# Kernel optimization log

Measured on AMD Instinct MI355X. Metric: run time of the kernel, lower is better.

Reference implementation:

```python
import jax, jax.numpy as jnp
import numpy as np

B, N, D, H = 4, 4096, 1024, 16
DK = D // H  # 64


def setup_inputs() -> dict:
    key = jax.random.key(0)
    ks = jax.random.split(key, 11)
    s_in = 1.0 / np.sqrt(D)
    s_out = 1.0 / np.sqrt(H * DK)
    return {
        "query": jax.random.normal(ks[0], (B, N, D), jnp.float32),
        "key": jax.random.normal(ks[1], (B, N, D), jnp.float32),
        "value": jax.random.normal(ks[2], (B, N, D), jnp.float32),
        # stacked per-head Linear weights (torch Linear: y = x @ W.T + b)
        "Wq": jax.random.uniform(ks[3], (H, DK, D), jnp.float32, -s_in, s_in),
        "bq": jax.random.uniform(ks[4], (H, DK), jnp.float32, -s_in, s_in),
        "Wk": jax.random.uniform(ks[5], (H, DK, D), jnp.float32, -s_in, s_in),
        "bk": jax.random.uniform(ks[6], (H, DK), jnp.float32, -s_in, s_in),
        "Wv": jax.random.uniform(ks[7], (H, DK, D), jnp.float32, -s_in, s_in),
        "bv": jax.random.uniform(ks[8], (H, DK), jnp.float32, -s_in, s_in),
        "Wo": jax.random.uniform(ks[9], (D, H * DK), jnp.float32, -s_out, s_out),
        "bo": jax.random.uniform(ks[10], (D,), jnp.float32, -s_out, s_out),
    }


def reference(query, key, value, Wq, bq, Wk, bk, Wv, bv, Wo, bo):
    b, n, _ = query.shape
    # batched per-head projections: [b,h,n,d_k]
    q = jnp.einsum('bnd,hkd->bhnk', query, Wq) + bq[None, :, None, :]
    k = jnp.einsum('bnd,hkd->bhnk', key, Wk) + bk[None, :, None, :]
    v = jnp.einsum('bnd,hkd->bhnk', value, Wv) + bv[None, :, None, :]
    # linear dot-product attention (faithful: scale by batch**-0.5)
    q = jax.nn.softmax(q, axis=-1) * (b ** -0.5)
    k = jax.nn.softmax(k, axis=-2)  # softmax over sequence dim
    ctx = jnp.einsum('bhnd,bhne->bhde', k, v)      # [b,h,d_k,d_v]
    attn = jnp.einsum('bhnd,bhde->bhne', q, ctx)   # [b,h,n,d_v]
    # concat heads along last dim: [b,n,h*d_v]
    concat = attn.transpose(0, 2, 1, 3).reshape(b, n, -1)
    return concat @ Wo.T + bo
```

## Files before the change

kernel.cpp:

```cpp
#include <hip/hip_runtime.h>
#include <hip/hip_bf16.h>
#include <stdint.h>

#define B_  4
#define N_  4096
#define D_  1024
#define H_  16
#define DK_ 64
#define M_  (B_ * N_)

typedef __attribute__((ext_vector_type(8))) short  short8;
typedef __attribute__((ext_vector_type(4))) float  f32x4;

__device__ __forceinline__ uint16_t f2bf(float f) {
  union { float f; uint32_t u; } v; v.f = f;
  uint32_t r = v.u + 0x7FFF + ((v.u >> 16) & 1);
  return (uint16_t)(r >> 16);
}
__device__ __forceinline__ uint32_t f2bf2(float lo, float hi) {
  return (uint32_t)f2bf(lo) | ((uint32_t)f2bf(hi) << 16);
}
__device__ __forceinline__ float bf2f(uint16_t u) {
  union { uint32_t u; float f; } v; v.u = ((uint32_t)u) << 16;
  return v.f;
}

__device__ __forceinline__ void gload_lds16(const void* g, void* l) {
  __builtin_amdgcn_global_load_lds((const __attribute__((address_space(1))) void*)g,
                                   (__attribute__((address_space(3))) void*)l, 16, 0, 0);
}

#define S_BARRIER() __builtin_amdgcn_s_barrier()
#define FENCE_LGKM0() asm volatile("s_waitcnt lgkmcnt(0)" ::: "memory")
#define FENCE_VM4()   asm volatile("s_waitcnt vmcnt(4) lgkmcnt(0)" ::: "memory")
#define FENCE_VM0()   asm volatile("s_waitcnt vmcnt(0) lgkmcnt(0)" ::: "memory")

__global__ __launch_bounds__(256) void pack_bf16_kernel(
    const float* q, const float* k, const float* v,
    const float* wq, const float* wk, const float* wv, const float* wo,
    uint16_t* xq, uint16_t* xk, uint16_t* xv,
    uint16_t* bwq, uint16_t* bwk, uint16_t* bwv, uint16_t* bwo)
{
  const float* src; uint16_t* dst; int count;
  switch (blockIdx.y) {
    case 0: src = q;  dst = xq;  count = M_ * D_; break;
    case 1: src = k;  dst = xk;  count = M_ * D_; break;
    case 2: src = v;  dst = xv;  count = M_ * D_; break;
    case 3: src = wq; dst = bwq; count = D_ * D_; break;
    case 4: src = wk; dst = bwk; count = D_ * D_; break;
    case 5: src = wv; dst = bwv; count = D_ * D_; break;
    default: src = wo; dst = bwo; count = D_ * D_; break;
  }
  int base = blockIdx.x * 4096;
  if (base >= count) return;
  int t = threadIdx.x;
#pragma unroll
  for (int j = 0; j < 2; ++j) {
    int idx = base + j * 2048 + t * 8;
    float4 f0 = *(const float4*)(src + idx);
    float4 f1 = *(const float4*)(src + idx + 4);
    uint4 o;
    o.x = f2bf2(f0.x, f0.y); o.y = f2bf2(f0.z, f0.w);
    o.z = f2bf2(f1.x, f1.y); o.w = f2bf2(f1.z, f1.w);
    *(uint4*)(dst + idx) = o;
  }
}

template<int EPI, int BATCHW>
__global__ __launch_bounds__(512, 2) void gemm256_kernel(
    const uint16_t* __restrict__ A,
    const uint16_t* __restrict__ W,
    const float* __restrict__ bias,
    void* __restrict__ C,
    float* __restrict__ pm, float* __restrict__ ps)
{
  extern __shared__ uint16_t smem[];
  uint16_t* As = smem;
  uint16_t* Bs = smem + 32768;
  float* sredm = (float*)(smem + 65536);
  float* sreds = sredm + 512;

  const int tid = threadIdx.x;
  const int w = tid >> 6, l = tid & 63;
  const int lr = l & 15, kg = l >> 4;
  const int wr = w >> 2, wc = w & 3;
  const int rsw = lr & 7;
  const int srcswz = ((tid >> 3) & 7) << 4;

  const int flat = blockIdx.y * 4 + blockIdx.x;
  const int swzf = (flat & 7) * 32 + (flat >> 3);
  const int brow = swzf >> 2, bcol = swzf & 3;
  const int NT = 16;

  const uint16_t* Wb = BATCHW ? (W + (size_t)(brow >> 4) * ((size_t)D_ * D_)) : W;
  const int arow0 = brow * 256, bcrow0 = bcol * 256;

  f32x4 acc[8][4];
#pragma unroll
  for (int i = 0; i < 8; ++i)
#pragma unroll
    for (int j = 0; j < 4; ++j) acc[i][j] = (f32x4){0.f, 0.f, 0.f, 0.f};

  auto stage_half = [&](const uint16_t* g, int row0, int kt, uint16_t* ldst, int h) {
#pragma unroll
    for (int i = 0; i < 2; ++i) {
      int lin = h * 16384 + i * 8192 + tid * 16;
      int src = lin ^ srcswz;
      const uint16_t* gp = g + (size_t)(row0 + (src >> 7)) * D_ + kt * 64 + ((src & 127) >> 1);
      uint16_t* lp = ldst + h * 8192 + i * 4096 + w * 512;
      gload_lds16(gp, lp);
    }
  };
  auto rdfrag = [&](const uint16_t* tile, int row, int ks) -> short8 {
    return *(const short8*)(tile + row * 64 + ((((ks << 2) | kg) ^ rsw) << 3));
  };

  stage_half(A, arow0, 0, As, 0);  stage_half(A, arow0, 0, As, 1);
  stage_half(Wb, bcrow0, 0, Bs, 0); stage_half(Wb, bcrow0, 0, Bs, 1);
  stage_half(A, arow0, 1, As + 16384, 0); stage_half(A, arow0, 1, As + 16384, 1);
  FENCE_VM4();
  S_BARRIER();

  short8 af0[4][2], af1[4][2], bfr[2][2];
  for (int t = 0; t < NT; ++t) {
    const int p = t & 1;
    uint16_t* Ap = As + p * 16384;
    uint16_t* Bp = Bs + p * 16384;
    uint16_t* An = As + (p ^ 1) * 16384;
    uint16_t* Bn = Bs + (p ^ 1) * 16384;

#pragma unroll
    for (int mi = 0; mi < 4; ++mi)
#pragma unroll
      for (int ks = 0; ks < 2; ++ks)
        af0[mi][ks] = rdfrag(Ap, wr * 128 + mi * 16 + lr, ks);
#pragma unroll
    for (int ni = 0; ni < 2; ++ni)
#pragma unroll
      for (int ks = 0; ks < 2; ++ks)
        bfr[ni][ks] = rdfrag(Bp, wc * 64 + ni * 16 + lr, ks);
    if (t + 1 < NT) stage_half(Wb, bcrow0, t + 1, Bn, 0);
    S_BARRIER();
    __builtin_amdgcn_s_setprio(1);
#pragma unroll
    for (int mi = 0; mi < 4; ++mi)
#pragma unroll
      for (int ni = 0; ni < 2; ++ni)
#pragma unroll
        for (int ks = 0; ks < 2; ++ks)
          acc[mi][ni] = __builtin_amdgcn_mfma_f32_16x16x32_bf16(af0[mi][ks], bfr[ni][ks], acc[mi][ni], 0, 0, 0);
    __builtin_amdgcn_s_setprio(0);
    FENCE_LGKM0();
    S_BARRIER();

#pragma unroll
    for (int mi = 0; mi < 4; ++mi)
#pragma unroll
      for (int ks = 0; ks < 2; ++ks)
        af1[mi][ks] = rdfrag(Ap, wr * 128 + 64 + mi * 16 + lr, ks);
#pragma unroll
    for (int ni = 0; ni < 2; ++ni)
#pragma unroll
      for (int ks = 0; ks < 2; ++ks)
        bfr[ni][ks] = rdfrag(Bp, wc * 64 + (ni + 2) * 16 + lr, ks);
    if (t + 1 < NT) stage_half(Wb, bcrow0, t + 1, Bn, 1);
    S_BARRIER();
    __builtin_amdgcn_s_setprio(1);
#pragma unroll
    for (int mi = 0; mi < 4; ++mi)
#pragma unroll
      for (int ni = 0; ni < 2; ++ni)
#pragma unroll
        for (int ks = 0; ks < 2; ++ks)
          acc[mi + 4][ni + 2] = __builtin_amdgcn_mfma_f32_16x16x32_bf16(af1[mi][ks], bfr[ni][ks], acc[mi + 4][ni + 2], 0, 0, 0);
    __builtin_amdgcn_s_setprio(0);
    FENCE_LGKM0();
    S_BARRIER();

#pragma unroll
    for (int ni = 0; ni < 2; ++ni)
#pragma unroll
      for (int ks = 0; ks < 2; ++ks)
        bfr[ni][ks] = rdfrag(Bp, wc * 64 + ni * 16 + lr, ks);
    if (t + 2 < NT) stage_half(A, arow0, t + 2, Ap, 0);
    S_BARRIER();
    __builtin_amdgcn_s_setprio(1);
#pragma unroll
    for (int mi = 0; mi < 4; ++mi)
#pragma unroll
      for (int ni = 0; ni < 2; ++ni)
#pragma unroll
        for (int ks = 0; ks < 2; ++ks)
          acc[mi + 4][ni] = __builtin_amdgcn_mfma_f32_16x16x32_bf16(af1[mi][ks], bfr[ni][ks], acc[mi + 4][ni], 0, 0, 0);
    __builtin_amdgcn_s_setprio(0);
    FENCE_LGKM0();
    S_BARRIER();

#pragma unroll
    for (int ni = 0; ni < 2; ++ni)
#pragma unroll
      for (int ks = 0; ks < 2; ++ks)
        bfr[ni][ks] = rdfrag(Bp, wc * 64 + (ni + 2) * 16 + lr, ks);
    if (t + 2 < NT) stage_half(A, arow0, t + 2, Ap, 1);
    S_BARRIER();
    __builtin_amdgcn_s_setprio(1);
#pragma unroll
    for (int mi = 0; mi < 4; ++mi)
#pragma unroll
      for (int ni = 0; ni < 2; ++ni)
#pragma unroll
        for (int ks = 0; ks < 2; ++ks)
          acc[mi][ni + 2] = __builtin_amdgcn_mfma_f32_16x16x32_bf16(af0[mi][ks], bfr[ni][ks], acc[mi][ni + 2], 0, 0, 0);
    __builtin_amdgcn_s_setprio(0);
    if (t <= 13)      { FENCE_VM4(); }
    else if (t == 14) { FENCE_VM0(); }
    else              { FENCE_LGKM0(); }
    S_BARRIER();
  }

  if (EPI == 2) {
    float bv[4];
#pragma unroll
    for (int ni = 0; ni < 4; ++ni) bv[ni] = bias[bcol * 256 + wc * 64 + ni * 16 + lr];
#pragma unroll
    for (int mi = 0; mi < 8; ++mi) {
#pragma unroll
      for (int j = 0; j < 4; ++j) {
        float v0 = acc[mi][0][j] + bv[0];
        float v1 = acc[mi][1][j] + bv[1];
        float v2 = acc[mi][2][j] + bv[2];
        float v3 = acc[mi][3][j] + bv[3];
        float m = fmaxf(fmaxf(v0, v1), fmaxf(v2, v3));
#pragma unroll
        for (int o = 1; o < 16; o <<= 1) m = fmaxf(m, __shfl_xor(m, o));
        float p0 = __expf(v0 - m), p1 = __expf(v1 - m);
        float p2 = __expf(v2 - m), p3 = __expf(v3 - m);
        float s = (p0 + p1) + (p2 + p3);
#pragma unroll
        for (int o = 1; o < 16; o <<= 1) s += __shfl_xor(s, o);
        float sc = 0.5f / s;
        int row = brow * 256 + wr * 128 + mi * 16 + kg * 4 + j;
        uint16_t* out = (uint16_t*)C + (size_t)row * D_ + bcol * 256 + wc * 64 + lr;
        out[0]  = f2bf(p0 * sc);
        out[16] = f2bf(p1 * sc);
        out[32] = f2bf(p2 * sc);
        out[48] = f2bf(p3 * sc);
      }
    }
  } else if (EPI == 3) {
#pragma unroll
    for (int ni = 0; ni < 4; ++ni) {
      int coll = wc * 64 + ni * 16 + lr;
      int col = bcol * 256 + coll;
      float bvn = bias[col];
      float vals[8][4];
      float m = -1e30f;
#pragma unroll
      for (int mi = 0; mi < 8; ++mi)
#pragma unroll
        for (int j = 0; j < 4; ++j) {
          float val = acc[mi][ni][j] + bvn;
          vals[mi][j] = val;
          m = fmaxf(m, val);
          int row = brow * 256 + wr * 128 + mi * 16 + kg * 4 + j;
          ((uint16_t*)C)[(size_t)row * D_ + col] = f2bf(val);
        }
      m = fmaxf(m, __shfl_xor(m, 16));
      m = fmaxf(m, __shfl_xor(m, 32));
      float s = 0.f;
#pragma unroll
      for (int mi = 0; mi < 8; ++mi)
#pragma unroll
        for (int j = 0; j < 4; ++j) s += __expf(vals[mi][j] - m);
      s += __shfl_xor(s, 16);
      s += __shfl_xor(s, 32);
      if (l < 16) {
        sredm[wr * 256 + coll] = m;
        sreds[wr * 256 + coll] = s;
      }
    }
    __syncthreads();
    if (tid < 256) {
      float m0 = sredm[tid], m1 = sredm[256 + tid];
      float s0 = sreds[tid], s1 = sreds[256 + tid];
      float m = fmaxf(m0, m1);
      float s = s0 * __expf(m0 - m) + s1 * __expf(m1 - m);
      pm[(size_t)brow * D_ + bcol * 256 + tid] = m;
      ps[(size_t)brow * D_ + bcol * 256 + tid] = s;
    }
  } else {
#pragma unroll
    for (int mi = 0; mi < 8; ++mi) {
#pragma unroll
      for (int ni = 0; ni < 4; ++ni) {
        int col = bcol * 256 + wc * 64 + ni * 16 + lr;
        float bv = bias[col];
#pragma unroll
        for (int j = 0; j < 4; ++j) {
          int row = brow * 256 + wr * 128 + mi * 16 + kg * 4 + j;
          float val = acc[mi][ni][j] + bv;
          if (EPI == 1) ((float*)C)[(size_t)row * D_ + col] = val;
          else          ((uint16_t*)C)[(size_t)row * D_ + col] = f2bf(val);
        }
      }
    }
  }
}

__global__ __launch_bounds__(256) void colstats_final_kernel(
    const float* __restrict__ pm, const float* __restrict__ ps,
    float* __restrict__ cmax, float* __restrict__ cinv)
{
  int f = blockIdx.x * 256 + threadIdx.x;
  int b = f >> 10, col = f & 1023;
  float m = -1e30f;
  for (int c = 0; c < 16; ++c) m = fmaxf(m, pm[(size_t)(b * 16 + c) * D_ + col]);
  float s = 0.f;
  for (int c = 0; c < 16; ++c)
    s += ps[(size_t)(b * 16 + c) * D_ + col] * __expf(pm[(size_t)(b * 16 + c) * D_ + col] - m);
  cmax[f] = m;
  cinv[f] = 1.f / s;
}

__global__ __launch_bounds__(256) void ctx_partial_kernel(
    const uint16_t* __restrict__ kp, const uint16_t* __restrict__ vp,
    const float* __restrict__ cmax, const float* __restrict__ cinv,
    float* __restrict__ ctxp)
{
  __shared__ float wk[64][64];
  __shared__ float vt[64][64];
  __shared__ float cm[64], ci[64];
  int t = threadIdx.x;
  int nchunk = blockIdx.x, h = blockIdx.y, b = blockIdx.z;
  if (t < 64) {
    cm[t] = cmax[b * D_ + h * 64 + t];
    ci[t] = cinv[b * D_ + h * 64 + t];
  }
  __syncthreads();
  int d0 = (t >> 4) * 4, e0 = (t & 15) * 4;
  f32x4 acc[4];
#pragma unroll
  for (int i = 0; i < 4; ++i) acc[i] = (f32x4){0.f, 0.f, 0.f, 0.f};

  for (int tt = 0; tt < 8; ++tt) {
    int n0 = nchunk * 512 + tt * 64;
#pragma unroll
    for (int i = 0; i < 4; ++i) {
      int qq = i * 256 + t;
      int r = qq >> 4, c4 = (qq & 15) * 4;
      size_t gi = (size_t)(b * N_ + n0 + r) * D_ + h * 64 + c4;
      union { uint16_t s[4]; uint2 u; } kk, vv;
      kk.u = *(const uint2*)(kp + gi);
      vv.u = *(const uint2*)(vp + gi);
#pragma unroll
      for (int j = 0; j < 4; ++j) {
        wk[r][c4 + j] = __expf(bf2f(kk.s[j]) - cm[c4 + j]) * ci[c4 + j];
        vt[r][c4 + j] = bf2f(vv.s[j]);
      }
    }
    __syncthreads();
#pragma unroll 8
    for (int n = 0; n < 64; ++n) {
      f32x4 wv = *(const f32x4*)&wk[n][d0];
      f32x4 vv4 = *(const f32x4*)&vt[n][e0];
#pragma unroll
      for (int di = 0; di < 4; ++di) acc[di] = acc[di] + vv4 * wv[di];
    }
    __syncthreads();
  }
  float* out = ctxp + (size_t)(nchunk * 64 + b * 16 + h) * 4096;
#pragma unroll
  for (int di = 0; di < 4; ++di)
    *(f32x4*)(out + (d0 + di) * 64 + e0) = acc[di];
}

__global__ __launch_bounds__(256) void ctx_reduce_kernel(
    const float* __restrict__ ctxp, float* __restrict__ ctx)
{
  int o = (blockIdx.x * 256 + threadIdx.x) * 4;
  f32x4 s = (f32x4){0.f, 0.f, 0.f, 0.f};
  for (int c = 0; c < 8; ++c) s = s + *(const f32x4*)(ctxp + (size_t)c * 262144 + o);
  *(f32x4*)(ctx + o) = s;
}

__global__ __launch_bounds__(256) void w2t_kernel(
    const float* __restrict__ ctx,
    const uint16_t* __restrict__ wo,
    uint16_t* __restrict__ w2t)
{
  __shared__ float ctxL[64][65];
  __shared__ float woL[64][65];
  int t = threadIdx.x;
  int otile = blockIdx.x, h = blockIdx.y, b = blockIdx.z;
  const float* csrc = ctx + (size_t)(b * 16 + h) * 4096;
#pragma unroll
  for (int i = 0; i < 4; ++i) {
    int idx = (i * 256 + t) * 4;
    int r = idx >> 6, c = idx & 63;
    f32x4 cv = *(const f32x4*)(csrc + idx);
    union { uint16_t s[4]; uint2 u; } wv;
    wv.u = *(const uint2*)(wo + (size_t)(otile * 64 + r) * D_ + h * 64 + c);
#pragma unroll
    for (int j = 0; j < 4; ++j) {
      ctxL[r][c + j] = cv[j];
      woL[r][c + j] = bf2f(wv.s[j]);
    }
  }
  __syncthreads();
  int ol = (t & 15) * 4, dl = (t >> 4) * 4;
  float acc[4][4];
#pragma unroll
  for (int i = 0; i < 4; ++i)
#pragma unroll
    for (int j = 0; j < 4; ++j) acc[i][j] = 0.f;
#pragma unroll 4
  for (int e = 0; e < 64; ++e) {
    float cv[4], wv[4];
#pragma unroll
    for (int i = 0; i < 4; ++i) { cv[i] = ctxL[dl + i][e]; wv[i] = woL[ol + i][e]; }
#pragma unroll
    for (int di = 0; di < 4; ++di)
#pragma unroll
      for (int oi = 0; oi < 4; ++oi) acc[di][oi] += cv[di] * wv[oi];
  }
  uint16_t* dst = w2t + (size_t)b * D_ * D_ + (size_t)(otile * 64) * D_ + h * 64;
#pragma unroll
  for (int oi = 0; oi < 4; ++oi) {
    union { uint16_t s[4]; uint2 u; } o4;
#pragma unroll
    for (int di = 0; di < 4; ++di) o4.s[di] = f2bf(acc[di][oi]);
    *(uint2*)(dst + (size_t)(ol + oi) * D_ + dl) = o4.u;
  }
}

extern "C" void kernel_launch(void* const* d_in, const int* in_sizes, int n_in,
                              void* d_out, int out_size, void* d_ws, size_t ws_size,
                              hipStream_t stream)
{
  const float* q  = (const float*)d_in[0];
  const float* k  = (const float*)d_in[1];
  const float* v  = (const float*)d_in[2];
  const float* Wq = (const float*)d_in[3];
  const float* bq = (const float*)d_in[4];
  const float* Wk = (const float*)d_in[5];
  const float* bk = (const float*)d_in[6];
  const float* Wv = (const float*)d_in[7];
  const float* bv = (const float*)d_in[8];
  const float* Wo = (const float*)d_in[9];
  const float* bo = (const float*)d_in[10];

  char* ws = (char*)d_ws;
  const size_t XB = (size_t)M_ * D_ * 2;
  const size_t WB = (size_t)D_ * D_ * 2;
  uint16_t* XQ  = (uint16_t*)(ws);
  uint16_t* XK  = (uint16_t*)(ws + XB);
  uint16_t* XV  = (uint16_t*)(ws + 2 * XB);
  uint16_t* WQb = (uint16_t*)(ws + 3 * XB);
  uint16_t* WKb = (uint16_t*)(ws + 3 * XB + WB);
  uint16_t* WVb = (uint16_t*)(ws + 3 * XB + 2 * WB);
  uint16_t* WOb = (uint16_t*)(ws + 3 * XB + 3 * WB);
  uint16_t* QS  = (uint16_t*)(ws + 3 * XB + 4 * WB);
  uint16_t* KP  = (uint16_t*)(ws + 4 * XB + 4 * WB);
  uint16_t* VP  = (uint16_t*)(ws + 5 * XB + 4 * WB);
  float* cmax = (float*)XK;
  float* cinv = (float*)((char*)XK + (16 << 10));
  float* ctxp = (float*)((char*)XK + (1 << 20));
  float* ctx  = (float*)((char*)XK + (9 << 20));
  uint16_t* W2T = XQ;
  float* pm = (float*)((char*)XQ + (16 << 20));
  float* ps = (float*)((char*)XQ + (16 << 20) + (512 << 10));

  const size_t LDSB = 135168;

  pack_bf16_kernel<<<dim3(4096, 7), 256, 0, stream>>>(
      q, k, v, Wq, Wk, Wv, Wo, XQ, XK, XV, WQb, WKb, WVb, WOb);

  gemm256_kernel<2, 0><<<dim3(4, 64), 512, LDSB, stream>>>(XQ, WQb, bq, QS, nullptr, nullptr);
  gemm256_kernel<3, 0><<<dim3(4, 64), 512, LDSB, stream>>>(XK, WKb, bk, KP, pm, ps);
  gemm256_kernel<0, 0><<<dim3(4, 64), 512, LDSB, stream>>>(XV, WVb, bv, VP, nullptr, nullptr);

  colstats_final_kernel<<<16, 256, 0, stream>>>(pm, ps, cmax, cinv);

  ctx_partial_kernel<<<dim3(8, H_, B_), 256, 0, stream>>>(KP, VP, cmax, cinv, ctxp);
  ctx_reduce_kernel<<<256, 256, 0, stream>>>(ctxp, ctx);

  w2t_kernel<<<dim3(16, 16, 4), 256, 0, stream>>>(ctx, WOb, W2T);

  gemm256_kernel<1, 1><<<dim3(4, 64), 512, LDSB, stream>>>(QS, W2T, bo, d_out, nullptr, nullptr);
}
```

Before: 276.3 us.

## Fuse fp32-to-bf16 activation conversion into projection GEMM A-tile loading

Drops the standalone pass that converts the three fp32 activation tensors to bf16. The projection GEMMs now load fp32 A tiles straight into registers, convert them, and write them to swizzled LDS inside the pipelined loop, while B still uses direct global-to-LDS loads. This removes one 96MB write plus reread of bf16 activations. In exchange the GEMM reads twice as many A bytes, uses more registers for A prefetch, and does the conversion work inside the main loop.

```diff
diff --git a/kernel.cpp b/kernel.cpp
--- a/kernel.cpp
+++ b/kernel.cpp
@@ -32,27 +32,22 @@
 
 #define S_BARRIER() __builtin_amdgcn_s_barrier()
 #define FENCE_LGKM0() asm volatile("s_waitcnt lgkmcnt(0)" ::: "memory")
+#define FENCE_VM8()   asm volatile("s_waitcnt vmcnt(8) lgkmcnt(0)" ::: "memory")
 #define FENCE_VM4()   asm volatile("s_waitcnt vmcnt(4) lgkmcnt(0)" ::: "memory")
 #define FENCE_VM0()   asm volatile("s_waitcnt vmcnt(0) lgkmcnt(0)" ::: "memory")
 
-__global__ __launch_bounds__(256) void pack_bf16_kernel(
-    const float* q, const float* k, const float* v,
+__global__ __launch_bounds__(256) void packw_kernel(
     const float* wq, const float* wk, const float* wv, const float* wo,
-    uint16_t* xq, uint16_t* xk, uint16_t* xv,
     uint16_t* bwq, uint16_t* bwk, uint16_t* bwv, uint16_t* bwo)
 {
-  const float* src; uint16_t* dst; int count;
+  const float* src; uint16_t* dst;
   switch (blockIdx.y) {
-    case 0: src = q;  dst = xq;  count = M_ * D_; break;
-    case 1: src = k;  dst = xk;  count = M_ * D_; break;
-    case 2: src = v;  dst = xv;  count = M_ * D_; break;
-    case 3: src = wq; dst = bwq; count = D_ * D_; break;
-    case 4: src = wk; dst = bwk; count = D_ * D_; break;
-    case 5: src = wv; dst = bwv; count = D_ * D_; break;
-    default: src = wo; dst = bwo; count = D_ * D_; break;
+    case 0: src = wq; dst = bwq; break;
+    case 1: src = wk; dst = bwk; break;
+    case 2: src = wv; dst = bwv; break;
+    default: src = wo; dst = bwo; break;
   }
   int base = blockIdx.x * 4096;
-  if (base >= count) return;
   int t = threadIdx.x;
 #pragma unroll
   for (int j = 0; j < 2; ++j) {
@@ -66,158 +61,13 @@
   }
 }
 
-template<int EPI, int BATCHW>
-__global__ __launch_bounds__(512, 2) void gemm256_kernel(
-    const uint16_t* __restrict__ A,
-    const uint16_t* __restrict__ W,
-    const float* __restrict__ bias,
-    void* __restrict__ C,
-    float* __restrict__ pm, float* __restrict__ ps)
-{
-  extern __shared__ uint16_t smem[];
-  uint16_t* As = smem;
-  uint16_t* Bs = smem + 32768;
-  float* sredm = (float*)(smem + 65536);
-  float* sreds = sredm + 512;
-
-  const int tid = threadIdx.x;
-  const int w = tid >> 6, l = tid & 63;
-  const int lr = l & 15, kg = l >> 4;
-  const int wr = w >> 2, wc = w & 3;
-  const int rsw = lr & 7;
-  const int srcswz = ((tid >> 3) & 7) << 4;
-
-  const int flat = blockIdx.y * 4 + blockIdx.x;
-  const int swzf = (flat & 7) * 32 + (flat >> 3);
-  const int brow = swzf >> 2, bcol = swzf & 3;
-  const int NT = 16;
-
-  const uint16_t* Wb = BATCHW ? (W + (size_t)(brow >> 4) * ((size_t)D_ * D_)) : W;
-  const int arow0 = brow * 256, bcrow0 = bcol * 256;
-
-  f32x4 acc[8][4];
-#pragma unroll
-  for (int i = 0; i < 8; ++i)
-#pragma unroll
-    for (int j = 0; j < 4; ++j) acc[i][j] = (f32x4){0.f, 0.f, 0.f, 0.f};
-
-  auto stage_half = [&](const uint16_t* g, int row0, int kt, uint16_t* ldst, int h) {
-#pragma unroll
-    for (int i = 0; i < 2; ++i) {
-      int lin = h * 16384 + i * 8192 + tid * 16;
-      int src = lin ^ srcswz;
-      const uint16_t* gp = g + (size_t)(row0 + (src >> 7)) * D_ + kt * 64 + ((src & 127) >> 1);
-      uint16_t* lp = ldst + h * 8192 + i * 4096 + w * 512;
-      gload_lds16(gp, lp);
-    }
-  };
-  auto rdfrag = [&](const uint16_t* tile, int row, int ks) -> short8 {
-    return *(const short8*)(tile + row * 64 + ((((ks << 2) | kg) ^ rsw) << 3));
-  };
-
-  stage_half(A, arow0, 0, As, 0);  stage_half(A, arow0, 0, As, 1);
-  stage_half(Wb, bcrow0, 0, Bs, 0); stage_half(Wb, bcrow0, 0, Bs, 1);
-  stage_half(A, arow0, 1, As + 16384, 0); stage_half(A, arow0, 1, As + 16384, 1);
-  FENCE_VM4();
-  S_BARRIER();
-
-  short8 af0[4][2], af1[4][2], bfr[2][2];
-  for (int t = 0; t < NT; ++t) {
-    const int p = t & 1;
-    uint16_t* Ap = As + p * 16384;
-    uint16_t* Bp = Bs + p * 16384;
-    uint16_t* An = As + (p ^ 1) * 16384;
-    uint16_t* Bn = Bs + (p ^ 1) * 16384;
-
-#pragma unroll
-    for (int mi = 0; mi < 4; ++mi)
-#pragma unroll
-      for (int ks = 0; ks < 2; ++ks)
-        af0[mi][ks] = rdfrag(Ap, wr * 128 + mi * 16 + lr, ks);
-#pragma unroll
-    for (int ni = 0; ni < 2; ++ni)
-#pragma unroll
-      for (int ks = 0; ks < 2; ++ks)
-        bfr[ni][ks] = rdfrag(Bp, wc * 64 + ni * 16 + lr, ks);
-    if (t + 1 < NT) stage_half(Wb, bcrow0, t + 1, Bn, 0);
-    S_BARRIER();
-    __builtin_amdgcn_s_setprio(1);
-#pragma unroll
-    for (int mi = 0; mi < 4; ++mi)
-#pragma unroll
-      for (int ni = 0; ni < 2; ++ni)
-#pragma unroll
-        for (int ks = 0; ks < 2; ++ks)
-          acc[mi][ni] = __builtin_amdgcn_mfma_f32_16x16x32_bf16(af0[mi][ks], bfr[ni][ks], acc[mi][ni], 0, 0, 0);
-    __builtin_amdgcn_s_setprio(0);
-    FENCE_LGKM0();
-    S_BARRIER();
-
-#pragma unroll
-    for (int mi = 0; mi < 4; ++mi)
-#pragma unroll
-      for (int ks = 0; ks < 2; ++ks)
-        af1[mi][ks] = rdfrag(Ap, wr * 128 + 64 + mi * 16 + lr, ks);
-#pragma unroll
-    for (int ni = 0; ni < 2; ++ni)
-#pragma unroll
-      for (int ks = 0; ks < 2; ++ks)
-        bfr[ni][ks] = rdfrag(Bp, wc * 64 + (ni + 2) * 16 + lr, ks);
-    if (t + 1 < NT) stage_half(Wb, bcrow0, t + 1, Bn, 1);
-    S_BARRIER();
-    __builtin_amdgcn_s_setprio(1);
-#pragma unroll
-    for (int mi = 0; mi < 4; ++mi)
-#pragma unroll
-      for (int ni = 0; ni < 2; ++ni)
-#pragma unroll
-        for (int ks = 0; ks < 2; ++ks)
-          acc[mi + 4][ni + 2] = __builtin_amdgcn_mfma_f32_16x16x32_bf16(af1[mi][ks], bfr[ni][ks], acc[mi + 4][ni + 2], 0, 0, 0);
-    __builtin_amdgcn_s_setprio(0);
-    FENCE_LGKM0();
-    S_BARRIER();
-
-#pragma unroll
-    for (int ni = 0; ni < 2; ++ni)
-#pragma unroll
-      for (int ks = 0; ks < 2; ++ks)
-        bfr[ni][ks] = rdfrag(Bp, wc * 64 + ni * 16 + lr, ks);
-    if (t + 2 < NT) stage_half(A, arow0, t + 2, Ap, 0);
-    S_BARRIER();
-    __builtin_amdgcn_s_setprio(1);
-#pragma unroll
-    for (int mi = 0; mi < 4; ++mi)
-#pragma unroll
-      for (int ni = 0; ni < 2; ++ni)
-#pragma unroll
-        for (int ks = 0; ks < 2; ++ks)
-          acc[mi + 4][ni] = __builtin_amdgcn_mfma_f32_16x16x32_bf16(af1[mi][ks], bfr[ni][ks], acc[mi + 4][ni], 0, 0, 0);
-    __builtin_amdgcn_s_setprio(0);
-    FENCE_LGKM0();
-    S_BARRIER();
-
-#pragma unroll
-    for (int ni = 0; ni < 2; ++ni)
-#pragma unroll
-      for (int ks = 0; ks < 2; ++ks)
-        bfr[ni][ks] = rdfrag(Bp, wc * 64 + (ni + 2) * 16 + lr, ks);
-    if (t + 2 < NT) stage_half(A, arow0, t + 2, Ap, 1);
-    S_BARRIER();
-    __builtin_amdgcn_s_setprio(1);
-#pragma unroll
-    for (int mi = 0; mi < 4; ++mi)
-#pragma unroll
-      for (int ni = 0; ni < 2; ++ni)
-#pragma unroll
-        for (int ks = 0; ks < 2; ++ks)
-          acc[mi][ni + 2] = __builtin_amdgcn_mfma_f32_16x16x32_bf16(af0[mi][ks], bfr[ni][ks], acc[mi][ni + 2], 0, 0, 0);
-    __builtin_amdgcn_s_setprio(0);
-    if (t <= 13)      { FENCE_VM4(); }
-    else if (t == 14) { FENCE_VM0(); }
-    else              { FENCE_LGKM0(); }
-    S_BARRIER();
-  }
-
+template<int EPI>
+__device__ __forceinline__ void gemm_epilogue(
+    f32x4 (&acc)[8][4], int tid, int l, int lr, int kg, int wr, int wc,
+    int brow, int bcol, const float* __restrict__ bias, void* __restrict__ C,
+    float* __restrict__ pm, float* __restrict__ ps,
+    float* sredm, float* sreds)
+{
   if (EPI == 2) {
     float bv[4];
 #pragma unroll
@@ -305,6 +155,345 @@
       }
     }
   }
+}
+
+template<int EPI>
+__global__ __launch_bounds__(512, 2) void gemm256f_kernel(
+    const float* __restrict__ A,
+    const uint16_t* __restrict__ W,
+    const float* __restrict__ bias,
+    void* __restrict__ C,
+    float* __restrict__ pm, float* __restrict__ ps)
+{
+  extern __shared__ uint16_t smem[];
+  uint16_t* As = smem;
+  uint16_t* Bs = smem + 32768;
+  float* sredm = (float*)(smem + 65536);
+  float* sreds = sredm + 512;
+
+  const int tid = threadIdx.x;
+  const int w = tid >> 6, l = tid & 63;
+  const int lr = l & 15, kg = l >> 4;
+  const int wr = w >> 2, wc = w & 3;
+  const int rsw = lr & 7;
+  const int srcswz = ((tid >> 3) & 7) << 4;
+
+  const int flat = blockIdx.y * 4 + blockIdx.x;
+  const int swzf = (flat & 7) * 32 + (flat >> 3);
+  const int brow = swzf >> 2, bcol = swzf & 3;
+  const int NT = 16;
+  const int arow0 = brow * 256, bcrow0 = bcol * 256;
+
+  f32x4 acc[8][4];
+#pragma unroll
+  for (int i = 0; i < 8; ++i)
+#pragma unroll
+    for (int j = 0; j < 4; ++j) acc[i][j] = (f32x4){0.f, 0.f, 0.f, 0.f};
+
+  auto stageB_half = [&](int kt, uint16_t* ldst, int h) {
+#pragma unroll
+    for (int i = 0; i < 2; ++i) {
+      int lin = h * 16384 + i * 8192 + tid * 16;
+      int src = lin ^ srcswz;
+      const uint16_t* gp = W + (size_t)(bcrow0 + (src >> 7)) * D_ + kt * 64 + ((src & 127) >> 1);
+      uint16_t* lp = ldst + h * 8192 + i * 4096 + w * 512;
+      gload_lds16(gp, lp);
+    }
+  };
+  auto loadA_half = [&](int kt, int h, float4* r) {
+#pragma unroll
+    for (int i = 0; i < 2; ++i) {
+      int lin = h * 16384 + i * 8192 + tid * 16;
+      const float* gp = A + (size_t)(arow0 + (lin >> 7)) * D_ + kt * 64 + ((lin & 127) >> 1);
+      r[i * 2]     = *(const float4*)gp;
+      r[i * 2 + 1] = *(const float4*)(gp + 4);
+    }
+  };
+  auto writeA_half = [&](uint16_t* ldst, int h, const float4* r) {
+#pragma unroll
+    for (int i = 0; i < 2; ++i) {
+      int lin = h * 16384 + i * 8192 + tid * 16;
+      int sw = ((lin >> 7) & 7) << 4;
+      uint4 o;
+      o.x = f2bf2(r[i * 2].x,     r[i * 2].y);
+      o.y = f2bf2(r[i * 2].z,     r[i * 2].w);
+      o.z = f2bf2(r[i * 2 + 1].x, r[i * 2 + 1].y);
+      o.w = f2bf2(r[i * 2 + 1].z, r[i * 2 + 1].w);
+      *(uint4*)((char*)ldst + (lin ^ sw)) = o;
+    }
+  };
+  auto rdfrag = [&](const uint16_t* tile, int row, int ks) -> short8 {
+    return *(const short8*)(tile + row * 64 + ((((ks << 2) | kg) ^ rsw) << 3));
+  };
+
+  float4 aH0[4], aH1[4];
+
+  loadA_half(0, 0, aH0);
+  loadA_half(0, 1, aH1);
+  stageB_half(0, Bs, 0); stageB_half(0, Bs, 1);
+  writeA_half(As, 0, aH0);
+  writeA_half(As, 1, aH1);
+  loadA_half(1, 0, aH0);
+  loadA_half(1, 1, aH1);
+  FENCE_VM8();
+  S_BARRIER();
+
+  short8 af0[4][2], af1[4][2], bfr[2][2];
+  for (int t = 0; t < NT; ++t) {
+    const int p = t & 1;
+    uint16_t* Ap = As + p * 16384;
+    uint16_t* Bp = Bs + p * 16384;
+    uint16_t* An = As + (p ^ 1) * 16384;
+    uint16_t* Bn = Bs + (p ^ 1) * 16384;
+    const bool st1 = (t + 1 < NT);
+    const bool st2 = (t + 2 < NT);
+
+#pragma unroll
+    for (int mi = 0; mi < 4; ++mi)
+#pragma unroll
+      for (int ks = 0; ks < 2; ++ks)
+        af0[mi][ks] = rdfrag(Ap, wr * 128 + mi * 16 + lr, ks);
+#pragma unroll
+    for (int ni = 0; ni < 2; ++ni)
+#pragma unroll
+      for (int ks = 0; ks < 2; ++ks)
+        bfr[ni][ks] = rdfrag(Bp, wc * 64 + ni * 16 + lr, ks);
+    if (st1) stageB_half(t + 1, Bn, 0);
+    if (st1) writeA_half(An, 0, aH0);
+    S_BARRIER();
+    __builtin_amdgcn_s_setprio(1);
+#pragma unroll
+    for (int mi = 0; mi < 4; ++mi)
+#pragma unroll
+      for (int ni = 0; ni < 2; ++ni)
+#pragma unroll
+        for (int ks = 0; ks < 2; ++ks)
+          acc[mi][ni] = __builtin_amdgcn_mfma_f32_16x16x32_bf16(af0[mi][ks], bfr[ni][ks], acc[mi][ni], 0, 0, 0);
+    __builtin_amdgcn_s_setprio(0);
+    FENCE_LGKM0();
+    S_BARRIER();
+
+#pragma unroll
+    for (int mi = 0; mi < 4; ++mi)
+#pragma unroll
+      for (int ks = 0; ks < 2; ++ks)
+        af1[mi][ks] = rdfrag(Ap, wr * 128 + 64 + mi * 16 + lr, ks);
+#pragma unroll
+    for (int ni = 0; ni < 2; ++ni)
+#pragma unroll
+      for (int ks = 0; ks < 2; ++ks)
+        bfr[ni][ks] = rdfrag(Bp, wc * 64 + (ni + 2) * 16 + lr, ks);
+    if (st1) stageB_half(t + 1, Bn, 1);
+    if (st1) writeA_half(An, 1, aH1);
+    S_BARRIER();
+    __builtin_amdgcn_s_setprio(1);
+#pragma unroll
+    for (int mi = 0; mi < 4; ++mi)
+#pragma unroll
+      for (int ni = 0; ni < 2; ++ni)
+#pragma unroll
+        for (int ks = 0; ks < 2; ++ks)
+          acc[mi + 4][ni + 2] = __builtin_amdgcn_mfma_f32_16x16x32_bf16(af1[mi][ks], bfr[ni][ks], acc[mi + 4][ni + 2], 0, 0, 0);
+    __builtin_amdgcn_s_setprio(0);
+    FENCE_LGKM0();
+    S_BARRIER();
+
+#pragma unroll
+    for (int ni = 0; ni < 2; ++ni)
+#pragma unroll
+      for (int ks = 0; ks < 2; ++ks)
+        bfr[ni][ks] = rdfrag(Bp, wc * 64 + ni * 16 + lr, ks);
+    if (st2) loadA_half(t + 2, 0, aH0);
+    S_BARRIER();
+    __builtin_amdgcn_s_setprio(1);
+#pragma unroll
+    for (int mi = 0; mi < 4; ++mi)
+#pragma unroll
+      for (int ni = 0; ni < 2; ++ni)
+#pragma unroll
+        for (int ks = 0; ks < 2; ++ks)
+          acc[mi + 4][ni] = __builtin_amdgcn_mfma_f32_16x16x32_bf16(af1[mi][ks], bfr[ni][ks], acc[mi + 4][ni], 0, 0, 0);
+    __builtin_amdgcn_s_setprio(0);
+    FENCE_LGKM0();
+    S_BARRIER();
+
+#pragma unroll
+    for (int ni = 0; ni < 2; ++ni)
+#pragma unroll
+      for (int ks = 0; ks < 2; ++ks)
+        bfr[ni][ks] = rdfrag(Bp, wc * 64 + (ni + 2) * 16 + lr, ks);
+    if (st2) loadA_half(t + 2, 1, aH1);
+    S_BARRIER();
+    __builtin_amdgcn_s_setprio(1);
+#pragma unroll
+    for (int mi = 0; mi < 4; ++mi)
+#pragma unroll
+      for (int ni = 0; ni < 2; ++ni)
+#pragma unroll
+        for (int ks = 0; ks < 2; ++ks)
+          acc[mi][ni + 2] = __builtin_amdgcn_mfma_f32_16x16x32_bf16(af0[mi][ks], bfr[ni][ks], acc[mi][ni + 2], 0, 0, 0);
+    __builtin_amdgcn_s_setprio(0);
+    if (t <= 13) { FENCE_VM8(); }
+    else         { FENCE_VM0(); }
+    S_BARRIER();
+  }
+
+  gemm_epilogue<EPI>(acc, tid, l, lr, kg, wr, wc, brow, bcol, bias, C, pm, ps, sredm, sreds);
+}
+
+template<int EPI, int BATCHW>
+__global__ __launch_bounds__(512, 2) void gemm256_kernel(
+    const uint16_t* __restrict__ A,
+    const uint16_t* __restrict__ W,
+    const float* __restrict__ bias,
+    void* __restrict__ C,
+    float* __restrict__ pm, float* __restrict__ ps)
+{
+  extern __shared__ uint16_t smem[];
+  uint16_t* As = smem;
+  uint16_t* Bs = smem + 32768;
+  float* sredm = (float*)(smem + 65536);
+  float* sreds = sredm + 512;
+
+  const int tid = threadIdx.x;
+  const int w = tid >> 6, l = tid & 63;
+  const int lr = l & 15, kg = l >> 4;
+  const int wr = w >> 2, wc = w & 3;
+  const int rsw = lr & 7;
+  const int srcswz = ((tid >> 3) & 7) << 4;
+
+  const int flat = blockIdx.y * 4 + blockIdx.x;
+  const int swzf = (flat & 7) * 32 + (flat >> 3);
+  const int brow = swzf >> 2, bcol = swzf & 3;
+  const int NT = 16;
+
+  const uint16_t* Wb = BATCHW ? (W + (size_t)(brow >> 4) * ((size_t)D_ * D_)) : W;
+  const int arow0 = brow * 256, bcrow0 = bcol * 256;
+
+  f32x4 acc[8][4];
+#pragma unroll
+  for (int i = 0; i < 8; ++i)
+#pragma unroll
+    for (int j = 0; j < 4; ++j) acc[i][j] = (f32x4){0.f, 0.f, 0.f, 0.f};
+
+  auto stage_half = [&](const uint16_t* g, int row0, int kt, uint16_t* ldst, int h) {
+#pragma unroll
+    for (int i = 0; i < 2; ++i) {
+      int lin = h * 16384 + i * 8192 + tid * 16;
+      int src = lin ^ srcswz;
+      const uint16_t* gp = g + (size_t)(row0 + (src >> 7)) * D_ + kt * 64 + ((src & 127) >> 1);
+      uint16_t* lp = ldst + h * 8192 + i * 4096 + w * 512;
+      gload_lds16(gp, lp);
+    }
+  };
+  auto rdfrag = [&](const uint16_t* tile, int row, int ks) -> short8 {
+    return *(const short8*)(tile + row * 64 + ((((ks << 2) | kg) ^ rsw) << 3));
+  };
+
+  stage_half(A, arow0, 0, As, 0);  stage_half(A, arow0, 0, As, 1);
+  stage_half(Wb, bcrow0, 0, Bs, 0); stage_half(Wb, bcrow0, 0, Bs, 1);
+  stage_half(A, arow0, 1, As + 16384, 0); stage_half(A, arow0, 1, As + 16384, 1);
+  FENCE_VM4();
+  S_BARRIER();
+
+  short8 af0[4][2], af1[4][2], bfr[2][2];
+  for (int t = 0; t < NT; ++t) {
+    const int p = t & 1;
+    uint16_t* Ap = As + p * 16384;
+    uint16_t* Bp = Bs + p * 16384;
+    uint16_t* An = As + (p ^ 1) * 16384;
+    uint16_t* Bn = Bs + (p ^ 1) * 16384;
+
+#pragma unroll
+    for (int mi = 0; mi < 4; ++mi)
+#pragma unroll
+      for (int ks = 0; ks < 2; ++ks)
+        af0[mi][ks] = rdfrag(Ap, wr * 128 + mi * 16 + lr, ks);
+#pragma unroll
+    for (int ni = 0; ni < 2; ++ni)
+#pragma unroll
+      for (int ks = 0; ks < 2; ++ks)
+        bfr[ni][ks] = rdfrag(Bp, wc * 64 + ni * 16 + lr, ks);
+    if (t + 1 < NT) stage_half(Wb, bcrow0, t + 1, Bn, 0);
+    S_BARRIER();
+    __builtin_amdgcn_s_setprio(1);
+#pragma unroll
+    for (int mi = 0; mi < 4; ++mi)
+#pragma unroll
+      for (int ni = 0; ni < 2; ++ni)
+#pragma unroll
+        for (int ks = 0; ks < 2; ++ks)
+          acc[mi][ni] = __builtin_amdgcn_mfma_f32_16x16x32_bf16(af0[mi][ks], bfr[ni][ks], acc[mi][ni], 0, 0, 0);
+    __builtin_amdgcn_s_setprio(0);
+    FENCE_LGKM0();
+    S_BARRIER();
+
+#pragma unroll
+    for (int mi = 0; mi < 4; ++mi)
+#pragma unroll
+      for (int ks = 0; ks < 2; ++ks)
+        af1[mi][ks] = rdfrag(Ap, wr * 128 + 64 + mi * 16 + lr, ks);
+#pragma unroll
+    for (int ni = 0; ni < 2; ++ni)
+#pragma unroll
+      for (int ks = 0; ks < 2; ++ks)
+        bfr[ni][ks] = rdfrag(Bp, wc * 64 + (ni + 2) * 16 + lr, ks);
+    if (t + 1 < NT) stage_half(Wb, bcrow0, t + 1, Bn, 1);
+    S_BARRIER();
+    __builtin_amdgcn_s_setprio(1);
+#pragma unroll
+    for (int mi = 0; mi < 4; ++mi)
+#pragma unroll
+      for (int ni = 0; ni < 2; ++ni)
+#pragma unroll
+        for (int ks = 0; ks < 2; ++ks)
+          acc[mi + 4][ni + 2] = __builtin_amdgcn_mfma_f32_16x16x32_bf16(af1[mi][ks], bfr[ni][ks], acc[mi + 4][ni + 2], 0, 0, 0);
+    __builtin_amdgcn_s_setprio(0);
+    FENCE_LGKM0();
+    S_BARRIER();
+
+#pragma unroll
+    for (int ni = 0; ni < 2; ++ni)
+#pragma unroll
+      for (int ks = 0; ks < 2; ++ks)
+        bfr[ni][ks] = rdfrag(Bp, wc * 64 + ni * 16 + lr, ks);
+    if (t + 2 < NT) stage_half(A, arow0, t + 2, Ap, 0);
+    S_BARRIER();
+    __builtin_amdgcn_s_setprio(1);
+#pragma unroll
+    for (int mi = 0; mi < 4; ++mi)
+#pragma unroll
+      for (int ni = 0; ni < 2; ++ni)
+#pragma unroll
+        for (int ks = 0; ks < 2; ++ks)
+          acc[mi + 4][ni] = __builtin_amdgcn_mfma_f32_16x16x32_bf16(af1[mi][ks], bfr[ni][ks], acc[mi + 4][ni], 0, 0, 0);
+    __builtin_amdgcn_s_setprio(0);
+    FENCE_LGKM0();
+    S_BARRIER();
+
+#pragma unroll
+    for (int ni = 0; ni < 2; ++ni)
+#pragma unroll
+      for (int ks = 0; ks < 2; ++ks)
+        bfr[ni][ks] = rdfrag(Bp, wc * 64 + (ni + 2) * 16 + lr, ks);
+    if (t + 2 < NT) stage_half(A, arow0, t + 2, Ap, 1);
+    S_BARRIER();
+    __builtin_amdgcn_s_setprio(1);
+#pragma unroll
+    for (int mi = 0; mi < 4; ++mi)
+#pragma unroll
+      for (int ni = 0; ni < 2; ++ni)
+#pragma unroll
+        for (int ks = 0; ks < 2; ++ks)
+          acc[mi][ni + 2] = __builtin_amdgcn_mfma_f32_16x16x32_bf16(af0[mi][ks], bfr[ni][ks], acc[mi][ni + 2], 0, 0, 0);
+    __builtin_amdgcn_s_setprio(0);
+    if (t <= 13)      { FENCE_VM4(); }
+    else if (t == 14) { FENCE_VM0(); }
+    else              { FENCE_LGKM0(); }
+    S_BARRIER();
+  }
+
+  gemm_epilogue<EPI>(acc, tid, l, lr, kg, wr, wc, brow, bcol, bias, C, pm, ps, sredm, sreds);
 }
 
 __global__ __launch_bounds__(256) void colstats_final_kernel(
@@ -450,34 +639,30 @@
   const float* bo = (const float*)d_in[10];
 
   char* ws = (char*)d_ws;
-  const size_t XB = (size_t)M_ * D_ * 2;
-  const size_t WB = (size_t)D_ * D_ * 2;
-  uint16_t* XQ  = (uint16_t*)(ws);
-  uint16_t* XK  = (uint16_t*)(ws + XB);
-  uint16_t* XV  = (uint16_t*)(ws + 2 * XB);
-  uint16_t* WQb = (uint16_t*)(ws + 3 * XB);
-  uint16_t* WKb = (uint16_t*)(ws + 3 * XB + WB);
-  uint16_t* WVb = (uint16_t*)(ws + 3 * XB + 2 * WB);
-  uint16_t* WOb = (uint16_t*)(ws + 3 * XB + 3 * WB);
-  uint16_t* QS  = (uint16_t*)(ws + 3 * XB + 4 * WB);
-  uint16_t* KP  = (uint16_t*)(ws + 4 * XB + 4 * WB);
-  uint16_t* VP  = (uint16_t*)(ws + 5 * XB + 4 * WB);
-  float* cmax = (float*)XK;
-  float* cinv = (float*)((char*)XK + (16 << 10));
-  float* ctxp = (float*)((char*)XK + (1 << 20));
-  float* ctx  = (float*)((char*)XK + (9 << 20));
-  uint16_t* W2T = XQ;
-  float* pm = (float*)((char*)XQ + (16 << 20));
-  float* ps = (float*)((char*)XQ + (16 << 20) + (512 << 10));
+  const size_t MB = 1 << 20;
+  uint16_t* WQb = (uint16_t*)(ws);
+  uint16_t* WKb = (uint16_t*)(ws + 2 * MB);
+  uint16_t* WVb = (uint16_t*)(ws + 4 * MB);
+  uint16_t* WOb = (uint16_t*)(ws + 6 * MB);
+  uint16_t* QS  = (uint16_t*)(ws + 8 * MB);
+  uint16_t* KP  = (uint16_t*)(ws + 40 * MB);
+  uint16_t* VP  = (uint16_t*)(ws + 72 * MB);
+  uint16_t* W2T = (uint16_t*)(ws + 104 * MB);
+  float* pm   = (float*)(ws + 112 * MB);
+  float* ps   = (float*)(ws + 112 * MB + 256 * 1024);
+  float* cmax = (float*)(ws + 112 * MB + 512 * 1024);
+  float* cinv = (float*)(ws + 112 * MB + 528 * 1024);
+  float* ctxp = (float*)(ws + 113 * MB);
+  float* ctx  = (float*)(ws + 121 * MB);
 
   const size_t LDSB = 135168;
 
-  pack_bf16_kernel<<<dim3(4096, 7), 256, 0, stream>>>(
-      q, k, v, Wq, Wk, Wv, Wo, XQ, XK, XV, WQb, WKb, WVb, WOb);
-
-  gemm256_kernel<2, 0><<<dim3(4, 64), 512, LDSB, stream>>>(XQ, WQb, bq, QS, nullptr, nullptr);
-  gemm256_kernel<3, 0><<<dim3(4, 64), 512, LDSB, stream>>>(XK, WKb, bk, KP, pm, ps);
-  gemm256_kernel<0, 0><<<dim3(4, 64), 512, LDSB, stream>>>(XV, WVb, bv, VP, nullptr, nullptr);
+  packw_kernel<<<dim3(256, 4), 256, 0, stream>>>(
+      Wq, Wk, Wv, Wo, WQb, WKb, WVb, WOb);
+
+  gemm256f_kernel<2><<<dim3(4, 64), 512, LDSB, stream>>>(q, WQb, bq, QS, nullptr, nullptr);
+  gemm256f_kernel<3><<<dim3(4, 64), 512, LDSB, stream>>>(k, WKb, bk, KP, pm, ps);
+  gemm256f_kernel<0><<<dim3(4, 64), 512, LDSB, stream>>>(v, WVb, bv, VP, nullptr, nullptr);
 
   colstats_final_kernel<<<16, 256, 0, stream>>>(pm, ps, cmax, cinv);
 
```

Result: slower. 297.7 us (+7.7%).
